# Kernel tuning notes

Measured on AMD Instinct MI355X. Metric: run time of the kernel, lower is better.

Reference implementation:

```python
import jax, jax.numpy as jnp
import numpy as np

WS = 8  # window size
NH = 4  # heads
EPS = 1e-5

def _rel_pos_index(ws):
    coords = np.stack(np.meshgrid(np.arange(ws), np.arange(ws), indexing='ij')).reshape(2, -1)
    rel = coords[:, :, None] - coords[:, None, :]
    rel[0] += ws - 1
    rel[1] += ws - 1
    rel[0] *= 2 * ws - 1
    return jnp.asarray(rel.sum(0))  # (ws*ws, ws*ws) int

REL_IDX = _rel_pos_index(WS)

def group_norm1(x, g, b):
    # GroupNorm(1, C): normalize over (C,H,W) per sample, per-channel affine
    m = jnp.mean(x, axis=(1, 2, 3), keepdims=True)
    v = jnp.var(x, axis=(1, 2, 3), keepdims=True)
    return (x - m) * jax.lax.rsqrt(v + EPS) * g[None, :, None, None] + b[None, :, None, None]

def conv1x1(x, w, b):
    return jnp.einsum('oc,bchw->bohw', w, x) + b[None, :, None, None]

def win_attn(x, qkv_w, qkv_b, out_w, out_b, bias_tab):
    # x: (B,H,W,C); non-shifted Swin window attention with gathered rel-pos bias
    B, H, W, C = x.shape
    hd = C // NH
    L = WS * WS
    scale = hd ** -0.5
    nh_, nw_ = H // WS, W // WS
    xw = x.reshape(B, nh_, WS, nw_, WS, C).transpose(0, 1, 3, 2, 4, 5).reshape(-1, L, C)
    qkv = (xw @ qkv_w.T + qkv_b).reshape(-1, L, 3, NH, hd)
    q = jnp.transpose(qkv[:, :, 0], (0, 2, 1, 3))  # (N,NH,L,hd)
    k = jnp.transpose(qkv[:, :, 1], (0, 2, 1, 3))
    v = jnp.transpose(qkv[:, :, 2], (0, 2, 1, 3))
    bias = bias_tab[:, REL_IDX.reshape(-1)].reshape(NH, L, L)
    attn = jax.nn.softmax(jnp.einsum('nhqd,nhkd->nhqk', q, k) * scale + bias[None], axis=-1)
    o = jnp.einsum('nhqk,nhkd->nhqd', attn, v).transpose(0, 2, 1, 3).reshape(-1, L, C)
    o = o @ out_w.T + out_b
    return o.reshape(B, nh_, nw_, WS, WS, C).transpose(0, 1, 3, 2, 4, 5).reshape(B, H, W, C)

def ffn(x, g, b, w1, b1, w2, b2):
    h = group_norm1(x, g, b)
    h = jax.nn.gelu(conv1x1(h, w1, b1), approximate=False)
    return conv1x1(h, w2, b2)

def setup_inputs() -> dict:
    key = jax.random.key(0)
    B, D, H, W = 8, 192, 128, 128
    ks = jax.random.split(key, 16)
    s = 0.02
    return {
        'sem': jax.random.normal(ks[0], (B, D, H, W), jnp.float32),
        'depth_feat': jax.random.normal(ks[1], (B, D, H, W), jnp.float32),
        'ns_g': jnp.ones((D,), jnp.float32), 'ns_b': jnp.zeros((D,), jnp.float32),
        'nd_g': jnp.ones((D,), jnp.float32), 'nd_b': jnp.zeros((D,), jnp.float32),
        'wd2s': jax.random.normal(ks[2], (D, D), jnp.float32) * s, 'bd2s': jnp.zeros((D,), jnp.float32),
        'ws2d': jax.random.normal(ks[3], (D, D), jnp.float32) * s, 'bs2d': jnp.zeros((D,), jnp.float32),
        'alpha': jnp.float32(0.1), 'beta': jnp.float32(0.1),
        'qkv_sem_w': jax.random.normal(ks[4], (3 * D, D), jnp.float32) * s, 'qkv_sem_b': jnp.zeros((3 * D,), jnp.float32),
        'out_sem_w': jax.random.normal(ks[5], (D, D), jnp.float32) * s, 'out_sem_b': jnp.zeros((D,), jnp.float32),
        'qkv_dep_w': jax.random.normal(ks[6], (3 * D, D), jnp.float32) * s, 'qkv_dep_b': jnp.zeros((3 * D,), jnp.float32),
        'out_dep_w': jax.random.normal(ks[7], (D, D), jnp.float32) * s, 'out_dep_b': jnp.zeros((D,), jnp.float32),
        'rel_pos_bias': jax.random.normal(ks[8], (NH, (2 * WS - 1) ** 2), jnp.float32) * s,
        'fs_g': jnp.ones((D,), jnp.float32), 'fs_b': jnp.zeros((D,), jnp.float32),
        'fs_w1': jax.random.normal(ks[9], (2 * D, D), jnp.float32) * s, 'fs_b1': jnp.zeros((2 * D,), jnp.float32),
        'fs_w2': jax.random.normal(ks[10], (D, 2 * D), jnp.float32) * s, 'fs_b2': jnp.zeros((D,), jnp.float32),
        'fd_g': jnp.ones((D,), jnp.float32), 'fd_b': jnp.zeros((D,), jnp.float32),
        'fd_w1': jax.random.normal(ks[11], (2 * D, D), jnp.float32) * s, 'fd_b1': jnp.zeros((2 * D,), jnp.float32),
        'fd_w2': jax.random.normal(ks[12], (D, 2 * D), jnp.float32) * s, 'fd_b2': jnp.zeros((D,), jnp.float32),
    }

def reference(sem, depth_feat, ns_g, ns_b, nd_g, nd_b, wd2s, bd2s, ws2d, bs2d, alpha, beta,
              qkv_sem_w, qkv_sem_b, out_sem_w, out_sem_b, qkv_dep_w, qkv_dep_b, out_dep_w, out_dep_b,
              rel_pos_bias, fs_g, fs_b, fs_w1, fs_b1, fs_w2, fs_b2, fd_g, fd_b, fd_w1, fd_b1, fd_w2, fd_b2):
    sem_n = group_norm1(sem, ns_g, ns_b)
    depth_n = group_norm1(depth_feat, nd_g, nd_b)
    sem_in = sem_n + alpha * jax.nn.sigmoid(conv1x1(depth_n, wd2s, bd2s))
    dep_in = depth_n + beta * jax.nn.sigmoid(conv1x1(sem_n, ws2d, bs2d))
    sem_hw = jnp.transpose(sem_in, (0, 2, 3, 1))  # (B,H,W,C)
    dep_hw = jnp.transpose(dep_in, (0, 2, 3, 1))
    sem_a = win_attn(sem_hw, qkv_sem_w, qkv_sem_b, out_sem_w, out_sem_b, rel_pos_bias)
    dep_a = win_attn(dep_hw, qkv_dep_w, qkv_dep_b, out_dep_w, out_dep_b, rel_pos_bias)
    sem_out = sem + jnp.transpose(sem_a, (0, 3, 1, 2))
    dep_out = depth_feat + jnp.transpose(dep_a, (0, 3, 1, 2))
    sem_out = sem_out + ffn(sem_out, fs_g, fs_b, fs_w1, fs_b1, fs_w2, fs_b2)
    dep_out = dep_out + ffn(dep_out, fd_g, fd_b, fd_w1, fd_b1, fd_w2, fd_b2)
    return (sem_out, dep_out)
```

## Files before the change

kernel.cpp:

```cpp
#include <hip/hip_runtime.h>

typedef unsigned short u16;
typedef float f32x4 __attribute__((ext_vector_type(4)));
typedef int   i32x4 __attribute__((ext_vector_type(4)));
typedef short bf16x8 __attribute__((ext_vector_type(8)));

#define CCH    192
#define HW     16384
#define NPIX   131072
#define NELEM  25165824
#define NSAMP  3145728

__device__ __forceinline__ float b2f(u16 u) {
  return __uint_as_float(((unsigned)u) << 16);
}
__device__ __forceinline__ u16 f2b(float f) {
  unsigned u = __float_as_uint(f);
  unsigned r = (u + 0x7fffu + ((u >> 16) & 1u)) >> 16;
  return (u16)r;
}
__device__ __forceinline__ void unpack8(i32x4 v, float* f) {
#pragma unroll
  for (int i = 0; i < 4; i++) {
    unsigned u = (unsigned)v[i];
    f[2 * i]     = __uint_as_float(u << 16);
    f[2 * i + 1] = __uint_as_float(u & 0xffff0000u);
  }
}
__device__ __forceinline__ i32x4 pack8(const float* f) {
  i32x4 r;
#pragma unroll
  for (int i = 0; i < 4; i++) {
    unsigned lo = f2b(f[2 * i]);
    unsigned hi = f2b(f[2 * i + 1]);
    r[i] = (int)(lo | (hi << 16));
  }
  return r;
}

__global__ __launch_bounds__(256) void stats_partial(
    const float* __restrict__ A, const float* __restrict__ B,
    float* __restrict__ acc, int slotbase) {
  const float* src = (blockIdx.z == 0) ? A : B;
  int sample = blockIdx.y;
  size_t base = (size_t)sample * NSAMP + (size_t)blockIdx.x * 32768;
  float s = 0.f, q = 0.f;
  for (int it = 0; it < 16; it++) {
    const float* ptr = src + base + it * 2048 + threadIdx.x * 8;
    f32x4 v0 = *(const f32x4*)ptr;
    f32x4 v1 = *(const f32x4*)(ptr + 4);
#pragma unroll
    for (int i = 0; i < 4; i++) {
      s += v0[i] + v1[i];
      q += v0[i] * v0[i] + v1[i] * v1[i];
    }
  }
#pragma unroll
  for (int o = 32; o > 0; o >>= 1) {
    s += __shfl_down(s, o);
    q += __shfl_down(q, o);
  }
  __shared__ float red[8];
  int wv = threadIdx.x >> 6;
  if ((threadIdx.x & 63) == 0) { red[wv * 2] = s; red[wv * 2 + 1] = q; }
  __syncthreads();
  if (threadIdx.x == 0) {
    float S = red[0] + red[2] + red[4] + red[6];
    float Q = red[1] + red[3] + red[5] + red[7];
    int e = ((slotbase + blockIdx.z) * 8 + sample) * 2;
    atomicAdd(&acc[e], S);
    atomicAdd(&acc[e + 1], Q);
  }
}

__global__ void finalize_stats(const float* __restrict__ acc,
                               float* __restrict__ mr, int entbase, int nent) {
  int i = threadIdx.x;
  if (i < nent) {
    int e = entbase + i;
    float s = acc[e * 2], q = acc[e * 2 + 1];
    const float invN = 1.0f / (float)NSAMP;
    float mean = s * invN;
    float var = q * invN - mean * mean;
    mr[e * 2] = mean;
    mr[e * 2 + 1] = rsqrtf(var + 1e-5f);
  }
}

__global__ __launch_bounds__(256) void norm_t(
    const float* __restrict__ in, u16* __restrict__ outp,
    const float* __restrict__ g, const float* __restrict__ bb,
    const float* __restrict__ mr, int slot) {
  __shared__ u16 tile[128 * 201];
  int yy = blockIdx.x, b = blockIdx.y;
  int e = (slot * 8 + b) * 2;
  float mean = mr[e], rstd = mr[e + 1];
  int tid = threadIdx.x;
  for (int task = tid; task < 3072; task += 256) {
    int c = task >> 4, xc = task & 15;
    const float* p = in + (size_t)(b * CCH + c) * HW + yy * 128 + xc * 8;
    f32x4 v0 = *(const f32x4*)p;
    f32x4 v1 = *(const f32x4*)(p + 4);
    float sc = rstd * g[c];
    float of = bb[c] - mean * sc;
#pragma unroll
    for (int i = 0; i < 4; i++) {
      tile[(xc * 8 + i) * 201 + c]       = f2b(v0[i] * sc + of);
      tile[(xc * 8 + 4 + i) * 201 + c]   = f2b(v1[i] * sc + of);
    }
  }
  __syncthreads();
  size_t ob = ((size_t)b * HW + (size_t)yy * 128) * CCH;
  for (int task = tid; task < 3072; task += 256) {
    int xx = task / 24, cc = task % 24;
    i32x4 v;
#pragma unroll
    for (int i = 0; i < 4; i++) {
      unsigned lo = tile[xx * 201 + cc * 8 + 2 * i];
      unsigned hi = tile[xx * 201 + cc * 8 + 2 * i + 1];
      v[i] = (int)(lo | (hi << 16));
    }
    *(i32x4*)(outp + ob + (size_t)xx * CCH + cc * 8) = v;
  }
}

__global__ void build_bias(const float* __restrict__ relb,
                           float* __restrict__ biasx) {
  int tid = threadIdx.x;
  for (int i = tid; i < 16384; i += 256) {
    int r    = i & 3;
    int lane = (i >> 2) & 63;
    int nj   = (i >> 8) & 3;
    int mi   = (i >> 10) & 3;
    int h    = (i >> 12) & 3;
    int q = 16 * mi + (lane >> 4) * 4 + r;
    int k = 16 * nj + (lane & 15);
    int qy = q >> 3, qx = q & 7, ky = k >> 3, kx = k & 7;
    biasx[i] = relb[h * 225 + (qy - ky + 7) * 15 + (qx - kx + 7)];
  }
}

__global__ __launch_bounds__(256) void attn_kernel(
    const u16* __restrict__ qkv, const float* __restrict__ biasx,
    u16* __restrict__ outp) {
  __shared__ u16 kp[4][64 * 72];
  __shared__ u16 vt[4][48 * 72];
  int tid = threadIdx.x;
  int h = tid >> 6, lane = tid & 63;
  int l15 = lane & 15, g4 = lane >> 4;
  int win = blockIdx.x;
  int b = win >> 8, wy = (win >> 4) & 15, wx = win & 15;
  int pbase = (b << 14) + (wy * 8) * 128 + wx * 8;

  for (int task = tid; task < 1536; task += 256) {
    int tok = task / 24;
    int r24 = task - tok * 24;
    int hh = r24 / 6;
    int c = r24 - hh * 6;
    int p = pbase + (tok >> 3) * 128 + (tok & 7);
    i32x4 v = *(const i32x4*)(qkv + (size_t)p * 576 + 192 + hh * 48 + c * 8);
    *(i32x4*)&kp[hh][tok * 72 + c * 8] = v;
  }
  {
    i32x4 z = {0, 0, 0, 0};
    for (int task = tid; task < 512; task += 256) {
      int hh = task >> 7, rem = task & 127, tok = rem >> 1, c = rem & 1;
      *(i32x4*)&kp[hh][tok * 72 + 48 + c * 8] = z;
    }
  }
  for (int task = tid; task < 1536; task += 256) {
    int chidx = task >> 6, tok = task & 63;
    int hh = chidx / 6, c = chidx - hh * 6;
    int p = pbase + (tok >> 3) * 128 + (tok & 7);
    i32x4 v = *(const i32x4*)(qkv + (size_t)p * 576 + 384 + hh * 48 + c * 8);
#pragma unroll
    for (int i = 0; i < 4; i++) {
      unsigned u = (unsigned)v[i];
      vt[hh][(c * 8 + 2 * i) * 72 + tok]     = (u16)(u & 0xffffu);
      vt[hh][(c * 8 + 2 * i + 1) * 72 + tok] = (u16)(u >> 16);
    }
  }
  __syncthreads();

  int ptok[4];
#pragma unroll
  for (int mi = 0; mi < 4; mi++) {
    int t = 16 * mi + l15;
    ptok[mi] = pbase + (t >> 3) * 128 + (t & 7);
  }
  f32x4 acc[4][4];
#pragma unroll
  for (int i = 0; i < 4; i++)
#pragma unroll
    for (int j = 0; j < 4; j++) {
      f32x4 z = {0.f, 0.f, 0.f, 0.f};
      acc[i][j] = z;
    }
#pragma unroll
  for (int s = 0; s < 2; s++) {
    bf16x8 qf[4], kf[4];
#pragma unroll
    for (int mi = 0; mi < 4; mi++)
      qf[mi] = *(const bf16x8*)(qkv + (size_t)ptok[mi] * 576 + h * 48 + s * 32 + g4 * 8);
#pragma unroll
    for (int nj = 0; nj < 4; nj++)
      kf[nj] = *(const bf16x8*)&kp[h][(16 * nj + l15) * 72 + s * 32 + g4 * 8];
#pragma unroll
    for (int mi = 0; mi < 4; mi++)
#pragma unroll
      for (int nj = 0; nj < 4; nj++)
        acc[mi][nj] = __builtin_amdgcn_mfma_f32_16x16x32_bf16(qf[mi], kf[nj], acc[mi][nj], 0, 0, 0);
  }

  const float scale = 0.14433756729740643f;
  float sums[4][4];
#pragma unroll
  for (int mi = 0; mi < 4; mi++) {
#pragma unroll
    for (int r = 0; r < 4; r++) sums[mi][r] = 0.f;
#pragma unroll
    for (int nj = 0; nj < 4; nj++) {
      f32x4 bv = *(const f32x4*)&biasx[(((h * 4 + mi) * 4 + nj) * 64 + lane) * 4];
#pragma unroll
      for (int r = 0; r < 4; r++) {
        float sv = acc[mi][nj][r] * scale + bv[r];
        sv = fminf(fmaxf(sv, -60.f), 60.f);
        float e = __expf(sv);
        acc[mi][nj][r] = e;
        sums[mi][r] += e;
      }
    }
  }
#pragma unroll
  for (int mi = 0; mi < 4; mi++)
#pragma unroll
    for (int r = 0; r < 4; r++) {
      float s = sums[mi][r];
      s += __shfl_xor(s, 1);
      s += __shfl_xor(s, 2);
      s += __shfl_xor(s, 4);
      s += __shfl_xor(s, 8);
      sums[mi][r] = 1.0f / s;
    }
#pragma unroll
  for (int mi = 0; mi < 4; mi++)
#pragma unroll
    for (int nj = 0; nj < 4; nj++)
#pragma unroll
      for (int r = 0; r < 4; r++)
        kp[h][(16 * mi + g4 * 4 + r) * 72 + 16 * nj + l15] = f2b(acc[mi][nj][r]);

  f32x4 oacc[4][3];
#pragma unroll
  for (int i = 0; i < 4; i++)
#pragma unroll
    for (int j = 0; j < 3; j++) {
      f32x4 z = {0.f, 0.f, 0.f, 0.f};
      oacc[i][j] = z;
    }
#pragma unroll
  for (int s = 0; s < 2; s++) {
    bf16x8 pf[4], vf[3];
#pragma unroll
    for (int mi = 0; mi < 4; mi++)
      pf[mi] = *(const bf16x8*)&kp[h][(16 * mi + l15) * 72 + s * 32 + g4 * 8];
#pragma unroll
    for (int n = 0; n < 3; n++)
      vf[n] = *(const bf16x8*)&vt[h][(16 * n + l15) * 72 + s * 32 + g4 * 8];
#pragma unroll
    for (int mi = 0; mi < 4; mi++)
#pragma unroll
      for (int n = 0; n < 3; n++)
        oacc[mi][n] = __builtin_amdgcn_mfma_f32_16x16x32_bf16(pf[mi], vf[n], oacc[mi][n], 0, 0, 0);
  }

#pragma unroll
  for (int mi = 0; mi < 4; mi++)
#pragma unroll
    for (int n = 0; n < 3; n++)
#pragma unroll
      for (int r = 0; r < 4; r++)
        kp[h][(16 * mi + g4 * 4 + r) * 72 + 16 * n + l15] =
            f2b(oacc[mi][n][r] * sums[mi][r]);
  __syncthreads();
  for (int task = tid; task < 1536; task += 256) {
    int tok = task / 24;
    int r24 = task - tok * 24;
    int hh = r24 / 6;
    int c = r24 - hh * 6;
    int p = pbase + (tok >> 3) * 128 + (tok & 7);
    *(i32x4*)(outp + (size_t)p * 192 + hh * 48 + c * 8) =
        *(const i32x4*)&kp[hh][tok * 72 + c * 8];
  }
}

enum { GM_BIAS = 0, GM_GATE = 1, GM_GELU = 2, GM_RES = 3 };

struct SmemGemm {
  union {
    struct { u16 xs[64 * 72]; u16 ws[64 * 72]; } s;
    float y[64 * 72];
  };
};

template <int MODE>
__global__ __launch_bounds__(256) void gemm_kernel(
    const u16* __restrict__ X, const float* __restrict__ W,
    const float* __restrict__ bias, const void* aux,
    void* outv, const float* __restrict__ scale_ptr, int K, int O) {
  __shared__ SmemGemm sm;
  int tid = threadIdx.x;
  int p0 = blockIdx.x * 64;
  int o0 = blockIdx.y * 64;
  int lane = tid & 63, wave = tid >> 6;
  int l15 = lane & 15, q8 = lane >> 4;
  int wm = (wave & 1) * 32, wn = (wave >> 1) * 32;

  f32x4 acc[2][2];
#pragma unroll
  for (int i = 0; i < 2; i++)
#pragma unroll
    for (int j = 0; j < 2; j++) {
      f32x4 z = {0.f, 0.f, 0.f, 0.f};
      acc[i][j] = z;
    }

  int srow = tid >> 2;
  int scol = (tid & 3) * 16;
  const u16* xg   = X + (size_t)(p0 + srow) * K + scol;
  const float* wg = W + (size_t)(o0 + srow) * K + scol;
  u16* xst = &sm.s.xs[srow * 72 + scol];
  u16* wst = &sm.s.ws[srow * 72 + scol];

  for (int k0 = 0; k0 < K; k0 += 64) {
    __syncthreads();
    i32x4 x0 = *(const i32x4*)xg;
    i32x4 x1 = *(const i32x4*)(xg + 8);
    f32x4 wv0 = *(const f32x4*)wg;
    f32x4 wv1 = *(const f32x4*)(wg + 4);
    f32x4 wv2 = *(const f32x4*)(wg + 8);
    f32x4 wv3 = *(const f32x4*)(wg + 12);
    xg += 64; wg += 64;
    float wf[16];
#pragma unroll
    for (int i = 0; i < 4; i++) {
      wf[i] = wv0[i]; wf[4 + i] = wv1[i]; wf[8 + i] = wv2[i]; wf[12 + i] = wv3[i];
    }
    *(i32x4*)xst = x0;
    *(i32x4*)(xst + 8) = x1;
    *(i32x4*)wst = pack8(wf);
    *(i32x4*)(wst + 8) = pack8(wf + 8);
    __syncthreads();
#pragma unroll
    for (int s = 0; s < 2; s++) {
      bf16x8 a0 = *(const bf16x8*)&sm.s.xs[(wm + l15) * 72 + s * 32 + q8 * 8];
      bf16x8 a1 = *(const bf16x8*)&sm.s.xs[(wm + 16 + l15) * 72 + s * 32 + q8 * 8];
      bf16x8 b0 = *(const bf16x8*)&sm.s.ws[(wn + l15) * 72 + s * 32 + q8 * 8];
      bf16x8 b1 = *(const bf16x8*)&sm.s.ws[(wn + 16 + l15) * 72 + s * 32 + q8 * 8];
      acc[0][0] = __builtin_amdgcn_mfma_f32_16x16x32_bf16(a0, b0, acc[0][0], 0, 0, 0);
      acc[0][1] = __builtin_amdgcn_mfma_f32_16x16x32_bf16(a0, b1, acc[0][1], 0, 0, 0);
      acc[1][0] = __builtin_amdgcn_mfma_f32_16x16x32_bf16(a1, b0, acc[1][0], 0, 0, 0);
      acc[1][1] = __builtin_amdgcn_mfma_f32_16x16x32_bf16(a1, b1, acc[1][1], 0, 0, 0);
    }
  }
  __syncthreads();
#pragma unroll
  for (int mi = 0; mi < 2; mi++) {
#pragma unroll
    for (int ni = 0; ni < 2; ni++) {
      int pl = wm + mi * 16 + q8 * 4;
      int ol = wn + ni * 16 + l15;
#pragma unroll
      for (int r = 0; r < 4; r++) {
        float v = acc[mi][ni][r];
        if (MODE == GM_RES) sm.y[ol * 72 + pl + r] = v;
        else                sm.y[(pl + r) * 72 + ol] = v;
      }
    }
  }
  __syncthreads();
  if (MODE == GM_RES) {
    const float* auxf = (const float*)aux;
    float* outf = (float*)outv;
    int o = tid >> 2;
    int pc = (tid & 3) * 16;
    float vals[16];
#pragma unroll
    for (int i = 0; i < 16; i++) vals[i] = sm.y[o * 72 + pc + i];
    int og = o0 + o;
    int pg = p0 + pc;
    int bi = pg >> 14;
    int r = pg & (HW - 1);
    size_t idx = ((size_t)(bi * CCH + og) << 14) + r;
    float bv = bias[og];
    f32x4 res[4];
#pragma unroll
    for (int i = 0; i < 4; i++) res[i] = *(const f32x4*)(auxf + idx + i * 4);
#pragma unroll
    for (int i = 0; i < 4; i++) {
      f32x4 w;
#pragma unroll
      for (int j = 0; j < 4; j++) w[j] = res[i][j] + vals[i * 4 + j] + bv;
      *(f32x4*)(outf + idx + i * 4) = w;
    }
  } else {
    u16* outb = (u16*)outv;
    const u16* auxb = (const u16*)aux;
    int pl = tid >> 2;
    int oc = (tid & 3) * 16;
    float vals[16];
#pragma unroll
    for (int i = 0; i < 16; i++) vals[i] = sm.y[pl * 72 + oc + i];
    int og0 = o0 + oc;
    size_t rowb = (size_t)(p0 + pl) * (size_t)O + og0;
    float sc = 0.f;
    if (MODE == GM_GATE) sc = scale_ptr[0];
    float f[16];
#pragma unroll
    for (int i = 0; i < 16; i++) {
      float v = vals[i] + bias[og0 + i];
      if (MODE == GM_GATE) {
        float sg = 1.0f / (1.0f + __expf(-v));
        v = b2f(auxb[rowb + i]) + sc * sg;
      } else if (MODE == GM_GELU) {
        v = 0.5f * v * (1.0f + erff(v * 0.70710678118654752f));
      }
      f[i] = v;
    }
    *(i32x4*)(outb + rowb) = pack8(f);
    *(i32x4*)(outb + rowb + 8) = pack8(f + 8);
  }
}

extern "C" void kernel_launch(void* const* d_in, const int* in_sizes, int n_in,
                              void* d_out, int out_size, void* d_ws,
                              size_t ws_size, hipStream_t stream) {
  (void)in_sizes; (void)n_in; (void)out_size; (void)ws_size;
  const float* sem       = (const float*)d_in[0];
  const float* dep       = (const float*)d_in[1];
  const float* ns_g      = (const float*)d_in[2];
  const float* ns_b      = (const float*)d_in[3];
  const float* nd_g      = (const float*)d_in[4];
  const float* nd_b      = (const float*)d_in[5];
  const float* wd2s      = (const float*)d_in[6];
  const float* bd2s      = (const float*)d_in[7];
  const float* ws2d      = (const float*)d_in[8];
  const float* bs2d      = (const float*)d_in[9];
  const float* alpha     = (const float*)d_in[10];
  const float* beta      = (const float*)d_in[11];
  const float* qkv_sem_w = (const float*)d_in[12];
  const float* qkv_sem_b = (const float*)d_in[13];
  const float* out_sem_w = (const float*)d_in[14];
  const float* out_sem_b = (const float*)d_in[15];
  const float* qkv_dep_w = (const float*)d_in[16];
  const float* qkv_dep_b = (const float*)d_in[17];
  const float* out_dep_w = (const float*)d_in[18];
  const float* out_dep_b = (const float*)d_in[19];
  const float* relb      = (const float*)d_in[20];
  const float* fs_g      = (const float*)d_in[21];
  const float* fs_b      = (const float*)d_in[22];
  const float* fs_w1     = (const float*)d_in[23];
  const float* fs_b1     = (const float*)d_in[24];
  const float* fs_w2     = (const float*)d_in[25];
  const float* fs_b2     = (const float*)d_in[26];
  const float* fd_g      = (const float*)d_in[27];
  const float* fd_b      = (const float*)d_in[28];
  const float* fd_w1     = (const float*)d_in[29];
  const float* fd_b1     = (const float*)d_in[30];
  const float* fd_w2     = (const float*)d_in[31];
  const float* fd_b2     = (const float*)d_in[32];

  float* stats_acc = (float*)d_ws;
  float* mr        = (float*)((char*)d_ws + 256);
  u16* R1 = (u16*)((char*)d_ws + 1024);
  u16* R2 = R1 + NELEM;
  u16* R3 = R2 + NELEM;
  u16* R4 = R3 + NELEM;
  u16* R5 = R4 + NELEM;
  float* outS = (float*)d_out;
  float* outD = outS + NELEM;
  float* biasx = (float*)R1;

  hipMemsetAsync(d_ws, 0, 512, stream);
  stats_partial<<<dim3(96, 8, 2), 256, 0, stream>>>(sem, dep, stats_acc, 0);
  finalize_stats<<<1, 64, 0, stream>>>(stats_acc, mr, 0, 16);
  norm_t<<<dim3(128, 8), 256, 0, stream>>>(sem, R1, ns_g, ns_b, mr, 0);
  norm_t<<<dim3(128, 8), 256, 0, stream>>>(dep, R2, nd_g, nd_b, mr, 1);
  gemm_kernel<GM_GATE><<<dim3(2048, 3), 256, 0, stream>>>(R2, wd2s, bd2s, R1, R3, alpha, 192, 192);
  gemm_kernel<GM_GATE><<<dim3(2048, 3), 256, 0, stream>>>(R1, ws2d, bs2d, R2, R4, beta, 192, 192);
  build_bias<<<1, 256, 0, stream>>>(relb, biasx);
  gemm_kernel<GM_BIAS><<<dim3(2048, 9), 256, 0, stream>>>(R3, qkv_sem_w, qkv_sem_b, nullptr, R5, nullptr, 192, 576);
  attn_kernel<<<2048, 256, 0, stream>>>(R5, biasx, R2);
  gemm_kernel<GM_RES><<<dim3(2048, 3), 256, 0, stream>>>(R2, out_sem_w, out_sem_b, sem, outS, nullptr, 192, 192);
  gemm_kernel<GM_BIAS><<<dim3(2048, 9), 256, 0, stream>>>(R4, qkv_dep_w, qkv_dep_b, nullptr, R5, nullptr, 192, 576);
  attn_kernel<<<2048, 256, 0, stream>>>(R5, biasx, R2);
  gemm_kernel<GM_RES><<<dim3(2048, 3), 256, 0, stream>>>(R2, out_dep_w, out_dep_b, dep, outD, nullptr, 192, 192);
  stats_partial<<<dim3(96, 8, 2), 256, 0, stream>>>(outS, outD, stats_acc, 2);
  finalize_stats<<<1, 64, 0, stream>>>(stats_acc, mr, 16, 16);
  norm_t<<<dim3(128, 8), 256, 0, stream>>>(outS, R1, fs_g, fs_b, mr, 2);
  norm_t<<<dim3(128, 8), 256, 0, stream>>>(outD, R3, fd_g, fd_b, mr, 3);
  gemm_kernel<GM_GELU><<<dim3(2048, 6), 256, 0, stream>>>(R1, fs_w1, fs_b1, nullptr, R5, nullptr, 192, 384);
  gemm_kernel<GM_RES><<<dim3(2048, 3), 256, 0, stream>>>(R5, fs_w2, fs_b2, outS, outS, nullptr, 384, 192);
  gemm_kernel<GM_GELU><<<dim3(2048, 6), 256, 0, stream>>>(R3, fd_w1, fd_b1, nullptr, R5, nullptr, 192, 384);
  gemm_kernel<GM_RES><<<dim3(2048, 3), 256, 0, stream>>>(R5, fd_w2, fd_b2, outD, outD, nullptr, 384, 192);
}
```

Baseline: 1.692 ms.

## Rewrite pointwise GEMMs with bf16 weights, direct fragment loads, and fused stats

```diff
diff --git a/kernel.cpp b/kernel.cpp
--- a/kernel.cpp
+++ b/kernel.cpp
@@ -140,6 +140,23 @@
   }
 }
 
+struct WPtrs { const float* p[10]; };
+
+__global__ __launch_bounds__(256) void convw(WPtrs wp, u16* __restrict__ dst) {
+  const int sz[10]  = {36864, 36864, 110592, 110592, 36864, 36864,
+                       73728, 73728, 73728, 73728};
+  const int off[10] = {0, 36864, 73728, 184320, 294912, 331776,
+                       368640, 442368, 516096, 589824};
+  int m = blockIdx.y;
+  int i = (blockIdx.x * 256 + threadIdx.x) * 8;
+  if (i >= sz[m]) return;
+  const float* s = wp.p[m];
+  f32x4 a = *(const f32x4*)(s + i);
+  f32x4 b = *(const f32x4*)(s + i + 4);
+  float f[8] = {a[0], a[1], a[2], a[3], b[0], b[1], b[2], b[3]};
+  *(i32x4*)(dst + off[m] + i) = pack8(f);
+}
+
 __global__ __launch_bounds__(256) void attn_kernel(
     const u16* __restrict__ qkv, const float* __restrict__ biasx,
     u16* __restrict__ outp) {
@@ -296,139 +313,145 @@
 
 enum { GM_BIAS = 0, GM_GATE = 1, GM_GELU = 2, GM_RES = 3 };
 
-struct SmemGemm {
-  union {
-    struct { u16 xs[64 * 72]; u16 ws[64 * 72]; } s;
-    float y[64 * 72];
-  };
-};
-
-template <int MODE>
-__global__ __launch_bounds__(256) void gemm_kernel(
-    const u16* __restrict__ X, const float* __restrict__ W,
-    const float* __restrict__ bias, const void* aux,
-    void* outv, const float* __restrict__ scale_ptr, int K, int O) {
-  __shared__ SmemGemm sm;
+template <int MODE, int KT>
+__global__ __launch_bounds__(256) void gemm2(
+    const u16* __restrict__ X, const u16* __restrict__ Wb,
+    const float* __restrict__ bias, const void* __restrict__ aux,
+    void* __restrict__ outv, const float* __restrict__ scale_ptr,
+    float* __restrict__ stats_acc, int statslot, int OB, int O) {
+  __shared__ float y[8704];
   int tid = threadIdx.x;
-  int p0 = blockIdx.x * 64;
-  int o0 = blockIdx.y * 64;
   int lane = tid & 63, wave = tid >> 6;
   int l15 = lane & 15, q8 = lane >> 4;
-  int wm = (wave & 1) * 32, wn = (wave >> 1) * 32;
-
-  f32x4 acc[2][2];
-#pragma unroll
-  for (int i = 0; i < 2; i++)
+  int wm = (wave & 1) * 64, wn = (wave >> 1) * 32;
+
+  int nwg = gridDim.x;
+  int cpx = nwg >> 3;
+  int bid = blockIdx.x;
+  int id = (bid & 7) * cpx + (bid >> 3);
+  int pt = id / OB;
+  int p0 = pt * 128;
+  int o0 = (id - pt * OB) * 64;
+
+  const u16* ax = X + (size_t)(p0 + wm + l15) * KT + q8 * 8;
+  const u16* bx = Wb + (size_t)(o0 + wn + l15) * KT + q8 * 8;
+
+  f32x4 acc[4][2];
+#pragma unroll
+  for (int i = 0; i < 4; i++)
 #pragma unroll
     for (int j = 0; j < 2; j++) {
       f32x4 z = {0.f, 0.f, 0.f, 0.f};
       acc[i][j] = z;
     }
 
-  int srow = tid >> 2;
-  int scol = (tid & 3) * 16;
-  const u16* xg   = X + (size_t)(p0 + srow) * K + scol;
-  const float* wg = W + (size_t)(o0 + srow) * K + scol;
-  u16* xst = &sm.s.xs[srow * 72 + scol];
-  u16* wst = &sm.s.ws[srow * 72 + scol];
-
-  for (int k0 = 0; k0 < K; k0 += 64) {
-    __syncthreads();
-    i32x4 x0 = *(const i32x4*)xg;
-    i32x4 x1 = *(const i32x4*)(xg + 8);
-    f32x4 wv0 = *(const f32x4*)wg;
-    f32x4 wv1 = *(const f32x4*)(wg + 4);
-    f32x4 wv2 = *(const f32x4*)(wg + 8);
-    f32x4 wv3 = *(const f32x4*)(wg + 12);
-    xg += 64; wg += 64;
-    float wf[16];
-#pragma unroll
-    for (int i = 0; i < 4; i++) {
-      wf[i] = wv0[i]; wf[4 + i] = wv1[i]; wf[8 + i] = wv2[i]; wf[12 + i] = wv3[i];
-    }
-    *(i32x4*)xst = x0;
-    *(i32x4*)(xst + 8) = x1;
-    *(i32x4*)wst = pack8(wf);
-    *(i32x4*)(wst + 8) = pack8(wf + 8);
-    __syncthreads();
-#pragma unroll
-    for (int s = 0; s < 2; s++) {
-      bf16x8 a0 = *(const bf16x8*)&sm.s.xs[(wm + l15) * 72 + s * 32 + q8 * 8];
-      bf16x8 a1 = *(const bf16x8*)&sm.s.xs[(wm + 16 + l15) * 72 + s * 32 + q8 * 8];
-      bf16x8 b0 = *(const bf16x8*)&sm.s.ws[(wn + l15) * 72 + s * 32 + q8 * 8];
-      bf16x8 b1 = *(const bf16x8*)&sm.s.ws[(wn + 16 + l15) * 72 + s * 32 + q8 * 8];
-      acc[0][0] = __builtin_amdgcn_mfma_f32_16x16x32_bf16(a0, b0, acc[0][0], 0, 0, 0);
-      acc[0][1] = __builtin_amdgcn_mfma_f32_16x16x32_bf16(a0, b1, acc[0][1], 0, 0, 0);
-      acc[1][0] = __builtin_amdgcn_mfma_f32_16x16x32_bf16(a1, b0, acc[1][0], 0, 0, 0);
-      acc[1][1] = __builtin_amdgcn_mfma_f32_16x16x32_bf16(a1, b1, acc[1][1], 0, 0, 0);
-    }
-  }
+  for (int kc = 0; kc < KT / 32; kc++) {
+    bf16x8 a0 = *(const bf16x8*)(ax);
+    bf16x8 a1 = *(const bf16x8*)(ax + 16 * KT);
+    bf16x8 a2 = *(const bf16x8*)(ax + 32 * KT);
+    bf16x8 a3 = *(const bf16x8*)(ax + 48 * KT);
+    bf16x8 b0 = *(const bf16x8*)(bx);
+    bf16x8 b1 = *(const bf16x8*)(bx + 16 * KT);
+    ax += 32; bx += 32;
+    acc[0][0] = __builtin_amdgcn_mfma_f32_16x16x32_bf16(a0, b0, acc[0][0], 0, 0, 0);
+    acc[0][1] = __builtin_amdgcn_mfma_f32_16x16x32_bf16(a0, b1, acc[0][1], 0, 0, 0);
+    acc[1][0] = __builtin_amdgcn_mfma_f32_16x16x32_bf16(a1, b0, acc[1][0], 0, 0, 0);
+    acc[1][1] = __builtin_amdgcn_mfma_f32_16x16x32_bf16(a1, b1, acc[1][1], 0, 0, 0);
+    acc[2][0] = __builtin_amdgcn_mfma_f32_16x16x32_bf16(a2, b0, acc[2][0], 0, 0, 0);
+    acc[2][1] = __builtin_amdgcn_mfma_f32_16x16x32_bf16(a2, b1, acc[2][1], 0, 0, 0);
+    acc[3][0] = __builtin_amdgcn_mfma_f32_16x16x32_bf16(a3, b0, acc[3][0], 0, 0, 0);
+    acc[3][1] = __builtin_amdgcn_mfma_f32_16x16x32_bf16(a3, b1, acc[3][1], 0, 0, 0);
+  }
+
+#pragma unroll
+  for (int mi = 0; mi < 4; mi++)
+#pragma unroll
+    for (int n = 0; n < 2; n++) {
+      int pl = wm + mi * 16 + q8 * 4;
+      int ol = wn + n * 16 + l15;
+      if (MODE == GM_RES) {
+        *(f32x4*)&y[ol * 132 + pl] = acc[mi][n];
+      } else {
+#pragma unroll
+        for (int r = 0; r < 4; r++) y[(pl + r) * 68 + ol] = acc[mi][n][r];
+      }
+    }
   __syncthreads();
-#pragma unroll
-  for (int mi = 0; mi < 2; mi++) {
-#pragma unroll
-    for (int ni = 0; ni < 2; ni++) {
-      int pl = wm + mi * 16 + q8 * 4;
-      int ol = wn + ni * 16 + l15;
-#pragma unroll
-      for (int r = 0; r < 4; r++) {
-        float v = acc[mi][ni][r];
-        if (MODE == GM_RES) sm.y[ol * 72 + pl + r] = v;
-        else                sm.y[(pl + r) * 72 + ol] = v;
-      }
-    }
-  }
-  __syncthreads();
+
   if (MODE == GM_RES) {
     const float* auxf = (const float*)aux;
     float* outf = (float*)outv;
-    int o = tid >> 2;
-    int pc = (tid & 3) * 16;
-    float vals[16];
-#pragma unroll
-    for (int i = 0; i < 16; i++) vals[i] = sm.y[o * 72 + pc + i];
-    int og = o0 + o;
-    int pg = p0 + pc;
-    int bi = pg >> 14;
-    int r = pg & (HW - 1);
-    size_t idx = ((size_t)(bi * CCH + og) << 14) + r;
+    int o2 = tid >> 2;
+    int pc = (tid & 3) * 32;
+    int og = o0 + o2;
+    int bi = p0 >> 14;
+    int r0 = (p0 + pc) & (HW - 1);
+    size_t idx = ((size_t)(bi * CCH + og) << 14) + r0;
     float bv = bias[og];
-    f32x4 res[4];
-#pragma unroll
-    for (int i = 0; i < 4; i++) res[i] = *(const f32x4*)(auxf + idx + i * 4);
-#pragma unroll
-    for (int i = 0; i < 4; i++) {
+    float s = 0.f, q = 0.f;
+#pragma unroll
+    for (int i = 0; i < 8; i++) {
+      f32x4 vy = *(const f32x4*)&y[o2 * 132 + pc + i * 4];
+      f32x4 av = *(const f32x4*)(auxf + idx + i * 4);
       f32x4 w;
 #pragma unroll
-      for (int j = 0; j < 4; j++) w[j] = res[i][j] + vals[i * 4 + j] + bv;
+      for (int j = 0; j < 4; j++) {
+        float t = av[j] + vy[j] + bv;
+        w[j] = t; s += t; q += t * t;
+      }
       *(f32x4*)(outf + idx + i * 4) = w;
     }
+    if (statslot >= 0) {
+#pragma unroll
+      for (int d = 32; d > 0; d >>= 1) {
+        s += __shfl_down(s, d);
+        q += __shfl_down(q, d);
+      }
+      if (lane == 0) {
+        int e = (statslot + bi) * 2;
+        atomicAdd(&stats_acc[e], s);
+        atomicAdd(&stats_acc[e + 1], q);
+      }
+    }
   } else {
+    int pl = tid >> 1;
+    int oc = (tid & 1) * 32;
+    float vals[32];
+#pragma unroll
+    for (int i = 0; i < 8; i++) {
+      f32x4 v = *(const f32x4*)&y[pl * 68 + oc + i * 4];
+      vals[i * 4] = v[0]; vals[i * 4 + 1] = v[1];
+      vals[i * 4 + 2] = v[2]; vals[i * 4 + 3] = v[3];
+    }
+    int og0 = o0 + oc;
+    size_t rowb = (size_t)(p0 + pl) * (size_t)O + og0;
     u16* outb = (u16*)outv;
     const u16* auxb = (const u16*)aux;
-    int pl = tid >> 2;
-    int oc = (tid & 3) * 16;
-    float vals[16];
-#pragma unroll
-    for (int i = 0; i < 16; i++) vals[i] = sm.y[pl * 72 + oc + i];
-    int og0 = o0 + oc;
-    size_t rowb = (size_t)(p0 + pl) * (size_t)O + og0;
     float sc = 0.f;
-    if (MODE == GM_GATE) sc = scale_ptr[0];
-    float f[16];
-#pragma unroll
-    for (int i = 0; i < 16; i++) {
+    float afv[32];
+    if (MODE == GM_GATE) {
+      sc = scale_ptr[0];
+#pragma unroll
+      for (int i = 0; i < 4; i++) {
+        i32x4 av = *(const i32x4*)(auxb + rowb + i * 8);
+        unpack8(av, &afv[i * 8]);
+      }
+    }
+    float f[32];
+#pragma unroll
+    for (int i = 0; i < 32; i++) {
       float v = vals[i] + bias[og0 + i];
       if (MODE == GM_GATE) {
         float sg = 1.0f / (1.0f + __expf(-v));
-        v = b2f(auxb[rowb + i]) + sc * sg;
+        v = afv[i] + sc * sg;
       } else if (MODE == GM_GELU) {
         v = 0.5f * v * (1.0f + erff(v * 0.70710678118654752f));
       }
       f[i] = v;
     }
-    *(i32x4*)(outb + rowb) = pack8(f);
-    *(i32x4*)(outb + rowb + 8) = pack8(f + 8);
+#pragma unroll
+    for (int i = 0; i < 4; i++)
+      *(i32x4*)(outb + rowb + i * 8) = pack8(&f[i * 8]);
   }
 }
 
@@ -477,30 +500,49 @@
   u16* R3 = R2 + NELEM;
   u16* R4 = R3 + NELEM;
   u16* R5 = R4 + NELEM;
+  u16* WB = R5 + (size_t)3 * NELEM;
   float* outS = (float*)d_out;
   float* outD = outS + NELEM;
   float* biasx = (float*)R1;
 
+  const u16* WD2S = WB;
+  const u16* WS2D = WB + 36864;
+  const u16* QKVS = WB + 73728;
+  const u16* QKVD = WB + 184320;
+  const u16* OUTS = WB + 294912;
+  const u16* OUTD = WB + 331776;
+  const u16* FSW1 = WB + 368640;
+  const u16* FDW1 = WB + 442368;
+  const u16* FSW2 = WB + 516096;
+  const u16* FDW2 = WB + 589824;
+
   hipMemsetAsync(d_ws, 0, 512, stream);
+  WPtrs wp;
+  wp.p[0] = wd2s;      wp.p[1] = ws2d;
+  wp.p[2] = qkv_sem_w; wp.p[3] = qkv_dep_w;
+  wp.p[4] = out_sem_w; wp.p[5] = out_dep_w;
+  wp.p[6] = fs_w1;     wp.p[7] = fd_w1;
+  wp.p[8] = fs_w2;     wp.p[9] = fd_w2;
+  convw<<<dim3(54, 10), 256, 0, stream>>>(wp, WB);
+
   stats_partial<<<dim3(96, 8, 2), 256, 0, stream>>>(sem, dep, stats_acc, 0);
   finalize_stats<<<1, 64, 0, stream>>>(stats_acc, mr, 0, 16);
   norm_t<<<dim3(128, 8), 256, 0, stream>>>(sem, R1, ns_g, ns_b, mr, 0);
   norm_t<<<dim3(128, 8), 256, 0, stream>>>(dep, R2, nd_g, nd_b, mr, 1);
-  gemm_kernel<GM_GATE><<<dim3(2048, 3), 256, 0, stream>>>(R2, wd2s, bd2s, R1, R3, alpha, 192, 192);
-  gemm_kernel<GM_GATE><<<dim3(2048, 3), 256, 0, stream>>>(R1, ws2d, bs2d, R2, R4, beta, 192, 192);
+  gemm2<GM_GATE, 192><<<3072, 256, 0, stream>>>(R2, WD2S, bd2s, R1, R3, alpha, nullptr, -1, 3, 192);
+  gemm2<GM_GATE, 192><<<3072, 256, 0, stream>>>(R1, WS2D, bs2d, R2, R4, beta, nullptr, -1, 3, 192);
   build_bias<<<1, 256, 0, stream>>>(relb, biasx);
-  gemm_kernel<GM_BIAS><<<dim3(2048, 9), 256, 0, stream>>>(R3, qkv_sem_w, qkv_sem_b, nullptr, R5, nullptr, 192, 576);
+  gemm2<GM_BIAS, 192><<<9216, 256, 0, stream>>>(R3, QKVS, qkv_sem_b, nullptr, R5, nullptr, nullptr, -1, 9, 576);
   attn_kernel<<<2048, 256, 0, stream>>>(R5, biasx, R2);
-  gemm_kernel<GM_RES><<<dim3(2048, 3), 256, 0, stream>>>(R2, out_sem_w, out_sem_b, sem, outS, nullptr, 192, 192);
-  gemm_kernel<GM_BIAS><<<dim3(2048, 9), 256, 0, stream>>>(R4, qkv_dep_w, qkv_dep_b, nullptr, R5, nullptr, 192, 576);
+  gemm2<GM_RES, 192><<<3072, 256, 0, stream>>>(R2, OUTS, out_sem_b, sem, outS, nullptr, stats_acc, 16, 3, 192);
+  gemm2<GM_BIAS, 192><<<9216, 256, 0, stream>>>(R4, QKVD, qkv_dep_b, nullptr, R5, nullptr, nullptr, -1, 9, 576);
   attn_kernel<<<2048, 256, 0, stream>>>(R5, biasx, R2);
-  gemm_kernel<GM_RES><<<dim3(2048, 3), 256, 0, stream>>>(R2, out_dep_w, out_dep_b, dep, outD, nullptr, 192, 192);
-  stats_partial<<<dim3(96, 8, 2), 256, 0, stream>>>(outS, outD, stats_acc, 2);
+  gemm2<GM_RES, 192><<<3072, 256, 0, stream>>>(R2, OUTD, out_dep_b, dep, outD, nullptr, stats_acc, 24, 3, 192);
   finalize_stats<<<1, 64, 0, stream>>>(stats_acc, mr, 16, 16);
   norm_t<<<dim3(128, 8), 256, 0, stream>>>(outS, R1, fs_g, fs_b, mr, 2);
   norm_t<<<dim3(128, 8), 256, 0, stream>>>(outD, R3, fd_g, fd_b, mr, 3);
-  gemm_kernel<GM_GELU><<<dim3(2048, 6), 256, 0, stream>>>(R1, fs_w1, fs_b1, nullptr, R5, nullptr, 192, 384);
-  gemm_kernel<GM_RES><<<dim3(2048, 3), 256, 0, stream>>>(R5, fs_w2, fs_b2, outS, outS, nullptr, 384, 192);
-  gemm_kernel<GM_GELU><<<dim3(2048, 6), 256, 0, stream>>>(R3, fd_w1, fd_b1, nullptr, R5, nullptr, 192, 384);
-  gemm_kernel<GM_RES><<<dim3(2048, 3), 256, 0, stream>>>(R5, fd_w2, fd_b2, outD, outD, nullptr, 384, 192);
-}
+  gemm2<GM_GELU, 192><<<6144, 256, 0, stream>>>(R1, FSW1, fs_b1, nullptr, R5, nullptr, nullptr, -1, 6, 384);
+  gemm2<GM_RES, 384><<<3072, 256, 0, stream>>>(R5, FSW2, fs_b2, outS, outS, nullptr, nullptr, -1, 3, 192);
+  gemm2<GM_GELU, 192><<<6144, 256, 0, stream>>>(R3, FDW1, fd_b1, nullptr, R5, nullptr, nullptr, -1, 6, 384);
+  gemm2<GM_RES, 384><<<3072, 256, 0, stream>>>(R5, FDW2, fd_b2, outD, outD, nullptr, nullptr, -1, 3, 192);
+}
```

Result: slower. 2.363 ms (+39.7%).
